# Performance work log

Measured on AMD Instinct MI355X. Metric: run time of the kernel, lower is better.

Reference implementation:

```python
import jax, jax.numpy as jnp
import numpy as np

N_SRC, N_DST, K = 50000, 10000, 32
IN_F, OUT_F, H, L = 256, 128, 8, 10


def setup_inputs() -> dict:
    key = jax.random.key(0)
    ks = jax.random.split(key, 12)
    s = 0.05
    return {
        "feat": jax.random.normal(ks[0], (N_SRC, IN_F), jnp.float32),
        "labels": jax.random.uniform(ks[1], (N_SRC, L), jnp.float32),
        "labels_ori": jax.random.uniform(ks[2], (N_SRC, L), jnp.float32),
        "label_rela": jax.random.uniform(ks[3], (L, L), jnp.float32),
        "W_neigh": jax.random.normal(ks[4], (IN_F, OUT_F), jnp.float32) * s,
        "b_neigh": jnp.zeros((OUT_F,), jnp.float32),
        "W_self": jax.random.normal(ks[5], (IN_F, OUT_F), jnp.float32) * s,
        "b_self": jnp.zeros((OUT_F,), jnp.float32),
        "W_attn": jax.random.normal(ks[6], (2 * OUT_F, OUT_F * H), jnp.float32) * s,
        "b_attn": jnp.zeros((OUT_F * H,), jnp.float32),
        "feat_attn_W": jax.random.normal(ks[7], (1, H, OUT_F), jnp.float32) * s,
        "eps": jnp.full((1,), 0.5, jnp.float32),
        "out_bias": jnp.zeros((OUT_F,), jnp.float32),
        "nbr_idx": jax.random.randint(ks[8], (N_DST, K), 0, N_SRC, jnp.int32),
    }


def reference(feat, labels, labels_ori, label_rela, W_neigh, b_neigh, W_self,
              b_self, W_attn, b_attn, feat_attn_W, eps, out_bias, nbr_idx):
    n_dst = nbr_idx.shape[0]
    # lin_before_mp is True (in_feats > out_feats): fc_neigh applied to src feats
    h_src = feat @ W_neigh + b_neigh                      # (N_SRC, OUT_F)
    feat_dst = feat[:n_dst]
    cent_l = labels[:n_dst]                                # dst predicted labels
    cent_f = h_src[:n_dst]                                 # dst 'f' field
    # mailbox gather: fixed-fanout neighbors
    h = h_src[nbr_idx]                                     # (N, K, OUT_F)
    l_pred = labels[nbr_idx]                               # (N, K, L)
    # label similarity: sum(outer(l_pred_j, cent_l_i) * R)
    label_sim = jnp.einsum('nka,ab,nb->nk', l_pred, label_rela, cent_l)
    # feature attention score
    h_act = jax.nn.leaky_relu(h, negative_slope=0.1)
    cent_rep = jnp.broadcast_to(cent_f[:, None, :], h_act.shape)
    x = jnp.concatenate([h_act, cent_rep], axis=-1)        # (N, K, 2*OUT_F)
    t = (x @ W_attn + b_attn).reshape(n_dst, K, H, OUT_F)
    feat_sim = jnp.einsum('nkhd,hd->nk', t, feat_attn_W[0])
    # merge (torch.tensor(...) in the original detaches this from the graph)
    merge = jax.lax.stop_gradient(label_sim * eps[0] + feat_sim * (1.0 - eps[0]))
    att = jax.nn.softmax(merge, axis=1)                    # (N, K)
    neigh = (h * att[:, :, None]).mean(axis=1)             # (N, OUT_F)
    rst = (feat_dst @ W_self + b_self + neigh) * 0.5 + out_bias
    return rst, cent_l, labels_ori[:n_dst]
```

## Files before the change

### kernel.cpp

```cpp
#include <hip/hip_runtime.h>
#include <hip/hip_bf16.h>

#define N_SRC 50000
#define N_DST 10000
#define KNBR  32
#define IN_F  256
#define OUT_F 128
#define LDIM  10
#define ATTN_OUT 1024
#define NB_BIG  782
#define NB_SELF 157

using f32x4 = __attribute__((ext_vector_type(4))) float;
using s16x8 = __attribute__((ext_vector_type(8))) short;

#define OUT_CENT (N_DST*OUT_F)
#define OUT_LORI (N_DST*OUT_F + N_DST*LDIM)

#define WS_WCOMB 0
#define WS_BN    128
#define WS_BS    (128 + 16384)
#define WS_HSRC  (128 + 32768)
#define WS_SELF0 (128 + 32768 + (N_SRC*OUT_F/2))
#define WS_SCORE (WS_SELF0 + N_DST*OUT_F)

__device__ __forceinline__ ushort f2bf(float x) {
  __hip_bfloat16 h = __float2bfloat16(x);
  return *reinterpret_cast<ushort*>(&h);
}

__global__ __launch_bounds__(256) void prep_kernel(
    const float* __restrict__ W_attn, const float* __restrict__ fW,
    const float* __restrict__ W_neigh, const float* __restrict__ W_self,
    float* __restrict__ w_comb, ushort* __restrict__ Bn, ushort* __restrict__ Bs) {
  const int b = blockIdx.x;
  const int t = threadIdx.x;
  if (b < 128) {
    __shared__ float red[256];
    float s = 0.f;
#pragma unroll
    for (int i = 0; i < 4; ++i) {
      int o = t + i * 256;
      s += W_attn[(size_t)b * ATTN_OUT + o] * fW[o];
    }
    red[t] = s;
    __syncthreads();
    for (int st = 128; st > 0; st >>= 1) {
      if (t < st) red[t] += red[t + st];
      __syncthreads();
    }
    if (t == 0) w_comb[b] = red[0];
  } else if (b < 256) {
    int k = 2 * (b - 128) + (t >> 7);
    int n = t & 127;
    float x = W_neigh[(size_t)k * OUT_F + n];
    Bn[(k >> 3) * 1024 + n * 8 + (k & 7)] = f2bf(x);
  } else {
    int k = 2 * (b - 256) + (t >> 7);
    int n = t & 127;
    float x = W_self[(size_t)k * OUT_F + n];
    Bs[(k >> 3) * 1024 + n * 8 + (k & 7)] = f2bf(x);
  }
}

template<bool OUT_BF16>
__device__ __forceinline__ void gemm_body(
    const float* __restrict__ A, const ushort* __restrict__ Bp,
    const float* __restrict__ bias, const float* __restrict__ w_comb,
    void* __restrict__ C, float* __restrict__ score_f, int M, int m0) {
  const int t = threadIdx.x;
  const int wv = t >> 6, ln = t & 63;
  const int dg = ln & 15, kg = ln >> 4;
  int r = m0 + wv * 16 + dg;
  r = r < M ? r : M - 1;
  const float* arow = &A[(size_t)r * IN_F];

  s16x8 afr[8];
#pragma unroll
  for (int half = 0; half < 2; ++half) {
    f32x4 araw[8];
#pragma unroll
    for (int k0 = 0; k0 < 4; ++k0) {
      const f32x4* ap = (const f32x4*)&arow[(half * 4 + k0) * 32 + kg * 8];
      araw[2 * k0]     = ap[0];
      araw[2 * k0 + 1] = ap[1];
    }
#pragma unroll
    for (int k0 = 0; k0 < 4; ++k0) {
      s16x8 f;
      f[0] = (short)f2bf(araw[2*k0][0]); f[1] = (short)f2bf(araw[2*k0][1]);
      f[2] = (short)f2bf(araw[2*k0][2]); f[3] = (short)f2bf(araw[2*k0][3]);
      f[4] = (short)f2bf(araw[2*k0+1][0]); f[5] = (short)f2bf(araw[2*k0+1][1]);
      f[6] = (short)f2bf(araw[2*k0+1][2]); f[7] = (short)f2bf(araw[2*k0+1][3]);
      afr[half * 4 + k0] = f;
    }
  }

  f32x4 acc[8];
#pragma unroll
  for (int ct = 0; ct < 8; ++ct) acc[ct] = (f32x4){0.f, 0.f, 0.f, 0.f};
#pragma unroll
  for (int k0 = 0; k0 < 8; ++k0) {
    const ushort* bb = Bp + (k0 * 4 + kg) * 1024 + dg * 8;
#pragma unroll
    for (int ct = 0; ct < 8; ++ct) {
      s16x8 bfr = *reinterpret_cast<const s16x8*>(bb + ct * 128);
      acc[ct] = __builtin_amdgcn_mfma_f32_16x16x32_bf16(afr[k0], bfr, acc[ct], 0, 0, 0);
    }
  }

  float sc[4] = {0.f, 0.f, 0.f, 0.f};
#pragma unroll
  for (int ct = 0; ct < 8; ++ct) {
    int col = ct * 16 + dg;
    float bb = bias[col];
    float wc = OUT_BF16 ? w_comb[col] : 0.f;
#pragma unroll
    for (int e = 0; e < 4; ++e) {
      int rr = m0 + wv * 16 + kg * 4 + e;
      float v = acc[ct][e] + bb;
      if (OUT_BF16) {
        sc[e] = fmaf(fmaxf(v, 0.1f * v), wc, sc[e]);
        if (rr < M) ((ushort*)C)[(size_t)rr * OUT_F + col] = f2bf(v);
      } else {
        if (rr < M) ((float*)C)[(size_t)rr * OUT_F + col] = v;
      }
    }
  }
  if (OUT_BF16) {
#pragma unroll
    for (int s = 1; s < 16; s <<= 1) {
#pragma unroll
      for (int e = 0; e < 4; ++e) sc[e] += __shfl_xor(sc[e], s);
    }
    if (dg == 0) {
#pragma unroll
      for (int e = 0; e < 4; ++e) {
        int rr = m0 + wv * 16 + kg * 4 + e;
        if (rr < M) score_f[rr] = sc[e];
      }
    }
  }
}

__global__ __launch_bounds__(256, 4) void fused_gemm(
    const float* __restrict__ A,
    const ushort* __restrict__ Bn, const ushort* __restrict__ Bs,
    const float* __restrict__ bias_n, const float* __restrict__ bias_s,
    const float* __restrict__ w_comb,
    ushort* __restrict__ hsrc, float* __restrict__ self0, float* __restrict__ score_f) {
  if (blockIdx.x < NB_BIG)
    gemm_body<true>(A, Bn, bias_n, w_comb, (void*)hsrc, score_f, N_SRC, blockIdx.x * 64);
  else
    gemm_body<false>(A, Bs, bias_s, w_comb, (void*)self0, score_f, N_DST, (blockIdx.x - NB_BIG) * 64);
}

__global__ __launch_bounds__(256, 4) void attn_kernel(
    const float* __restrict__ labels, const float* __restrict__ labels_ori,
    const float* __restrict__ label_rela, const int* __restrict__ nbr_idx,
    const ushort* __restrict__ hsrc, const float* __restrict__ self0,
    const float* __restrict__ score_f, const float* __restrict__ eps_p,
    const float* __restrict__ out_bias, float* __restrict__ out) {
  const int t = threadIdx.x;
  const int wv = t >> 6, ln = t & 63;
  const int n = blockIdx.x * 4 + wv;
  const int dg = ln & 15, kg = ln >> 4;

  const float eps = eps_p[0];
  const float om = 1.f - eps;

  float va = 0.f;
  if (dg < LDIM) {
#pragma unroll
    for (int b = 0; b < LDIM; ++b)
      va += label_rela[dg * LDIM + b] * labels[(size_t)n * LDIM + b];
    va *= eps;
  }

  const int* irow = nbr_idx + (size_t)n * KNBR;
  int ids[8];
  uint4 hv[8];
#pragma unroll
  for (int j = 0; j < 8; ++j) {
    ids[j] = irow[kg * 8 + j];
    hv[j] = *(const uint4*)(hsrc + (size_t)ids[j] * OUT_F + dg * 8);
  }
  float m[8];
#pragma unroll
  for (int j = 0; j < 8; ++j) {
    float sp = 0.f;
    if (dg == 0) sp = om * score_f[ids[j]];
    if (dg < LDIM) sp = fmaf(labels[(size_t)ids[j] * LDIM + dg], va, sp);
    m[j] = sp;
  }
#pragma unroll
  for (int s = 1; s < 16; s <<= 1) {
#pragma unroll
    for (int j = 0; j < 8; ++j) m[j] += __shfl_xor(m[j], s);
  }
  float mx = m[0];
#pragma unroll
  for (int j = 1; j < 8; ++j) mx = fmaxf(mx, m[j]);
  mx = fmaxf(mx, __shfl_xor(mx, 16));
  mx = fmaxf(mx, __shfl_xor(mx, 32));
  float ssum = 0.f;
#pragma unroll
  for (int j = 0; j < 8; ++j) {
    m[j] = __expf(m[j] - mx);
    ssum += m[j];
  }
  ssum += __shfl_xor(ssum, 16);
  ssum += __shfl_xor(ssum, 32);
  const float scale = 1.f / (ssum * (float)KNBR);
  float pn[8];
#pragma unroll
  for (int e = 0; e < 8; ++e) pn[e] = 0.f;
#pragma unroll
  for (int j = 0; j < 8; ++j) {
    float a = m[j];
    pn[0] = fmaf(a, __uint_as_float(hv[j].x << 16), pn[0]);
    pn[1] = fmaf(a, __uint_as_float(hv[j].x & 0xffff0000u), pn[1]);
    pn[2] = fmaf(a, __uint_as_float(hv[j].y << 16), pn[2]);
    pn[3] = fmaf(a, __uint_as_float(hv[j].y & 0xffff0000u), pn[3]);
    pn[4] = fmaf(a, __uint_as_float(hv[j].z << 16), pn[4]);
    pn[5] = fmaf(a, __uint_as_float(hv[j].z & 0xffff0000u), pn[5]);
    pn[6] = fmaf(a, __uint_as_float(hv[j].w << 16), pn[6]);
    pn[7] = fmaf(a, __uint_as_float(hv[j].w & 0xffff0000u), pn[7]);
  }
#pragma unroll
  for (int e = 0; e < 8; ++e) {
    pn[e] += __shfl_xor(pn[e], 16);
    pn[e] += __shfl_xor(pn[e], 32);
  }
  if (kg == 0) {
    const float* srow = self0 + (size_t)n * OUT_F + dg * 8;
    float* orow = out + (size_t)n * OUT_F + dg * 8;
    f32x4 o0, o1;
#pragma unroll
    for (int e = 0; e < 4; ++e)
      o0[e] = (srow[e] + pn[e] * scale) * 0.5f + out_bias[dg * 8 + e];
#pragma unroll
    for (int e = 0; e < 4; ++e)
      o1[e] = (srow[4 + e] + pn[4 + e] * scale) * 0.5f + out_bias[dg * 8 + 4 + e];
    *(f32x4*)orow = o0;
    *(f32x4*)(orow + 4) = o1;
  }
  if (kg == 1 && dg < LDIM)
    out[OUT_CENT + (size_t)n * LDIM + dg] = labels[(size_t)n * LDIM + dg];
  if (kg == 2 && dg < LDIM)
    out[OUT_LORI + (size_t)n * LDIM + dg] = labels_ori[(size_t)n * LDIM + dg];
}

extern "C" void kernel_launch(void* const* d_in, const int* in_sizes, int n_in,
                              void* d_out, int out_size, void* d_ws, size_t ws_size,
                              hipStream_t stream) {
  const float* feat       = (const float*)d_in[0];
  const float* labels     = (const float*)d_in[1];
  const float* labels_ori = (const float*)d_in[2];
  const float* label_rela = (const float*)d_in[3];
  const float* W_neigh    = (const float*)d_in[4];
  const float* b_neigh    = (const float*)d_in[5];
  const float* W_self     = (const float*)d_in[6];
  const float* b_self     = (const float*)d_in[7];
  const float* W_attn     = (const float*)d_in[8];
  const float* fW         = (const float*)d_in[10];
  const float* eps        = (const float*)d_in[11];
  const float* out_bias   = (const float*)d_in[12];
  const int*   nbr_idx    = (const int*)d_in[13];

  float* wsf = (float*)d_ws;
  float* out = (float*)d_out;

  float*  w_comb  = wsf + WS_WCOMB;
  ushort* Bn      = (ushort*)(wsf + WS_BN);
  ushort* Bsf     = (ushort*)(wsf + WS_BS);
  ushort* h_src   = (ushort*)(wsf + WS_HSRC);
  float*  self0   = wsf + WS_SELF0;
  float*  score_f = wsf + WS_SCORE;

  prep_kernel<<<384, 256, 0, stream>>>(W_attn, fW, W_neigh, W_self, w_comb, Bn, Bsf);
  fused_gemm<<<NB_BIG + NB_SELF, 256, 0, stream>>>(feat, Bn, Bsf, b_neigh, b_self,
                                                   w_comb, h_src, self0, score_f);
  attn_kernel<<<(N_DST / 4), 256, 0, stream>>>(labels, labels_ori, label_rela, nbr_idx,
                                               h_src, self0, score_f, eps, out_bias, out);
}
```

Measured before the change: 59.63 us.

## Split GEMM K dimension across wave pairs with LDS reduction, fold self epilogue

```diff
diff --git a/kernel.cpp b/kernel.cpp
--- a/kernel.cpp
+++ b/kernel.cpp
@@ -8,8 +8,9 @@
 #define OUT_F 128
 #define LDIM  10
 #define ATTN_OUT 1024
-#define NB_BIG  782
-#define NB_SELF 157
+#define NB2_BIG  1563
+#define NB2_SELF 313
+#define NB2_TOT  1876
 
 using f32x4 = __attribute__((ext_vector_type(4))) float;
 using s16x8 = __attribute__((ext_vector_type(8))) short;
@@ -21,12 +22,23 @@
 #define WS_BN    128
 #define WS_BS    (128 + 16384)
 #define WS_HSRC  (128 + 32768)
-#define WS_SELF0 (128 + 32768 + (N_SRC*OUT_F/2))
+#define WS_SELF0 (WS_HSRC + (N_SRC*OUT_F/2))
 #define WS_SCORE (WS_SELF0 + N_DST*OUT_F)
 
 __device__ __forceinline__ ushort f2bf(float x) {
   __hip_bfloat16 h = __float2bfloat16(x);
   return *reinterpret_cast<ushort*>(&h);
+}
+
+__device__ __forceinline__ void unpack8(uint4 hv, float* o) {
+  o[0] = __uint_as_float(hv.x << 16);
+  o[1] = __uint_as_float(hv.x & 0xffff0000u);
+  o[2] = __uint_as_float(hv.y << 16);
+  o[3] = __uint_as_float(hv.y & 0xffff0000u);
+  o[4] = __uint_as_float(hv.z << 16);
+  o[5] = __uint_as_float(hv.z & 0xffff0000u);
+  o[6] = __uint_as_float(hv.w << 16);
+  o[7] = __uint_as_float(hv.w & 0xffff0000u);
 }
 
 __global__ __launch_bounds__(256) void prep_kernel(
@@ -53,55 +65,52 @@
   } else if (b < 256) {
     int k = 2 * (b - 128) + (t >> 7);
     int n = t & 127;
-    float x = W_neigh[(size_t)k * OUT_F + n];
-    Bn[(k >> 3) * 1024 + n * 8 + (k & 7)] = f2bf(x);
+    Bn[(k >> 3) * 1024 + n * 8 + (k & 7)] = f2bf(W_neigh[(size_t)k * OUT_F + n]);
   } else {
     int k = 2 * (b - 256) + (t >> 7);
     int n = t & 127;
-    float x = W_self[(size_t)k * OUT_F + n];
-    Bs[(k >> 3) * 1024 + n * 8 + (k & 7)] = f2bf(x);
-  }
-}
-
-template<bool OUT_BF16>
-__device__ __forceinline__ void gemm_body(
-    const float* __restrict__ A, const ushort* __restrict__ Bp,
-    const float* __restrict__ bias, const float* __restrict__ w_comb,
-    void* __restrict__ C, float* __restrict__ score_f, int M, int m0) {
+    Bs[(k >> 3) * 1024 + n * 8 + (k & 7)] = f2bf(W_self[(size_t)k * OUT_F + n]);
+  }
+}
+
+template<bool NEIGH, bool SCORE>
+__device__ __forceinline__ void gemm_tile_ks(
+    const float* A, const ushort* Bp, const float* bias,
+    const float* out_bias, const float* w_comb, float* score_f,
+    void* C, int M, int m0) {
+  __shared__ f32x4 lred[2][64][8];
   const int t = threadIdx.x;
   const int wv = t >> 6, ln = t & 63;
+  const int grp = wv >> 1, half = wv & 1;
   const int dg = ln & 15, kg = ln >> 4;
-  int r = m0 + wv * 16 + dg;
+  int r = m0 + grp * 16 + dg;
   r = r < M ? r : M - 1;
-  const float* arow = &A[(size_t)r * IN_F];
-
-  s16x8 afr[8];
-#pragma unroll
-  for (int half = 0; half < 2; ++half) {
-    f32x4 araw[8];
-#pragma unroll
-    for (int k0 = 0; k0 < 4; ++k0) {
-      const f32x4* ap = (const f32x4*)&arow[(half * 4 + k0) * 32 + kg * 8];
-      araw[2 * k0]     = ap[0];
-      araw[2 * k0 + 1] = ap[1];
-    }
-#pragma unroll
-    for (int k0 = 0; k0 < 4; ++k0) {
-      s16x8 f;
-      f[0] = (short)f2bf(araw[2*k0][0]); f[1] = (short)f2bf(araw[2*k0][1]);
-      f[2] = (short)f2bf(araw[2*k0][2]); f[3] = (short)f2bf(araw[2*k0][3]);
-      f[4] = (short)f2bf(araw[2*k0+1][0]); f[5] = (short)f2bf(araw[2*k0+1][1]);
-      f[6] = (short)f2bf(araw[2*k0+1][2]); f[7] = (short)f2bf(araw[2*k0+1][3]);
-      afr[half * 4 + k0] = f;
-    }
+  const float* arow = &A[(size_t)r * IN_F + half * 128];
+
+  f32x4 araw[8];
+#pragma unroll
+  for (int k0 = 0; k0 < 4; ++k0) {
+    const f32x4* ap = (const f32x4*)&arow[k0 * 32 + kg * 8];
+    araw[2 * k0]     = ap[0];
+    araw[2 * k0 + 1] = ap[1];
+  }
+  s16x8 afr[4];
+#pragma unroll
+  for (int k0 = 0; k0 < 4; ++k0) {
+    s16x8 f;
+    f[0] = (short)f2bf(araw[2*k0][0]); f[1] = (short)f2bf(araw[2*k0][1]);
+    f[2] = (short)f2bf(araw[2*k0][2]); f[3] = (short)f2bf(araw[2*k0][3]);
+    f[4] = (short)f2bf(araw[2*k0+1][0]); f[5] = (short)f2bf(araw[2*k0+1][1]);
+    f[6] = (short)f2bf(araw[2*k0+1][2]); f[7] = (short)f2bf(araw[2*k0+1][3]);
+    afr[k0] = f;
   }
 
   f32x4 acc[8];
 #pragma unroll
   for (int ct = 0; ct < 8; ++ct) acc[ct] = (f32x4){0.f, 0.f, 0.f, 0.f};
 #pragma unroll
-  for (int k0 = 0; k0 < 8; ++k0) {
-    const ushort* bb = Bp + (k0 * 4 + kg) * 1024 + dg * 8;
+  for (int k0 = 0; k0 < 4; ++k0) {
+    const ushort* bb = Bp + (size_t)(half * 16 + k0 * 4 + kg) * 1024 + dg * 8;
 #pragma unroll
     for (int ct = 0; ct < 8; ++ct) {
       s16x8 bfr = *reinterpret_cast<const s16x8*>(bb + ct * 128);
@@ -109,35 +118,47 @@
     }
   }
 
-  float sc[4] = {0.f, 0.f, 0.f, 0.f};
-#pragma unroll
-  for (int ct = 0; ct < 8; ++ct) {
-    int col = ct * 16 + dg;
-    float bb = bias[col];
-    float wc = OUT_BF16 ? w_comb[col] : 0.f;
-#pragma unroll
-    for (int e = 0; e < 4; ++e) {
-      int rr = m0 + wv * 16 + kg * 4 + e;
-      float v = acc[ct][e] + bb;
-      if (OUT_BF16) {
-        sc[e] = fmaf(fmaxf(v, 0.1f * v), wc, sc[e]);
-        if (rr < M) ((ushort*)C)[(size_t)rr * OUT_F + col] = f2bf(v);
-      } else {
-        if (rr < M) ((float*)C)[(size_t)rr * OUT_F + col] = v;
+  if (half == 0) {
+#pragma unroll
+    for (int ct = 0; ct < 8; ++ct) lred[grp][ln][ct] = acc[ct];
+  }
+  __syncthreads();
+  if (half == 1) {
+#pragma unroll
+    for (int ct = 0; ct < 8; ++ct) {
+      f32x4 o = lred[grp][ln][ct];
+#pragma unroll
+      for (int e = 0; e < 4; ++e) acc[ct][e] += o[e];
+    }
+    float sc[4] = {0.f, 0.f, 0.f, 0.f};
+#pragma unroll
+    for (int ct = 0; ct < 8; ++ct) {
+      int col = ct * 16 + dg;
+      float bb = bias[col];
+      float wc = SCORE ? w_comb[col] : 0.f;
+#pragma unroll
+      for (int e = 0; e < 4; ++e) {
+        int rr = m0 + grp * 16 + kg * 4 + e;
+        float v = acc[ct][e] + bb;
+        if (SCORE) sc[e] = fmaf(fmaxf(v, 0.1f * v), wc, sc[e]);
+        if (rr < M) {
+          if (NEIGH) ((ushort*)C)[(size_t)rr * OUT_F + col] = f2bf(v);
+          else       ((float*)C)[(size_t)rr * OUT_F + col] = v * 0.5f + out_bias[col];
+        }
       }
     }
-  }
-  if (OUT_BF16) {
-#pragma unroll
-    for (int s = 1; s < 16; s <<= 1) {
-#pragma unroll
-      for (int e = 0; e < 4; ++e) sc[e] += __shfl_xor(sc[e], s);
-    }
-    if (dg == 0) {
-#pragma unroll
-      for (int e = 0; e < 4; ++e) {
-        int rr = m0 + wv * 16 + kg * 4 + e;
-        if (rr < M) score_f[rr] = sc[e];
+    if (SCORE) {
+#pragma unroll
+      for (int s = 1; s < 16; s <<= 1) {
+#pragma unroll
+        for (int e = 0; e < 4; ++e) sc[e] += __shfl_xor(sc[e], s);
+      }
+      if (dg == 0) {
+#pragma unroll
+        for (int e = 0; e < 4; ++e) {
+          int rr = m0 + grp * 16 + kg * 4 + e;
+          if (rr < M) score_f[rr] = sc[e];
+        }
       }
     }
   }
@@ -147,12 +168,14 @@
     const float* __restrict__ A,
     const ushort* __restrict__ Bn, const ushort* __restrict__ Bs,
     const float* __restrict__ bias_n, const float* __restrict__ bias_s,
-    const float* __restrict__ w_comb,
+    const float* __restrict__ w_comb, const float* __restrict__ out_bias,
     ushort* __restrict__ hsrc, float* __restrict__ self0, float* __restrict__ score_f) {
-  if (blockIdx.x < NB_BIG)
-    gemm_body<true>(A, Bn, bias_n, w_comb, (void*)hsrc, score_f, N_SRC, blockIdx.x * 64);
+  if (blockIdx.x < NB2_BIG)
+    gemm_tile_ks<true, true>(A, Bn, bias_n, out_bias, w_comb, score_f,
+                             (void*)hsrc, N_SRC, blockIdx.x * 32);
   else
-    gemm_body<false>(A, Bs, bias_s, w_comb, (void*)self0, score_f, N_DST, (blockIdx.x - NB_BIG) * 64);
+    gemm_tile_ks<false, false>(A, Bs, bias_s, out_bias, nullptr, nullptr,
+                               (void*)self0, N_DST, (blockIdx.x - NB2_BIG) * 32);
 }
 
 __global__ __launch_bounds__(256, 4) void attn_kernel(
@@ -211,21 +234,17 @@
   }
   ssum += __shfl_xor(ssum, 16);
   ssum += __shfl_xor(ssum, 32);
-  const float scale = 1.f / (ssum * (float)KNBR);
+  const float scale2 = 0.5f / (ssum * (float)KNBR);
   float pn[8];
 #pragma unroll
   for (int e = 0; e < 8; ++e) pn[e] = 0.f;
 #pragma unroll
   for (int j = 0; j < 8; ++j) {
     float a = m[j];
-    pn[0] = fmaf(a, __uint_as_float(hv[j].x << 16), pn[0]);
-    pn[1] = fmaf(a, __uint_as_float(hv[j].x & 0xffff0000u), pn[1]);
-    pn[2] = fmaf(a, __uint_as_float(hv[j].y << 16), pn[2]);
-    pn[3] = fmaf(a, __uint_as_float(hv[j].y & 0xffff0000u), pn[3]);
-    pn[4] = fmaf(a, __uint_as_float(hv[j].z << 16), pn[4]);
-    pn[5] = fmaf(a, __uint_as_float(hv[j].z & 0xffff0000u), pn[5]);
-    pn[6] = fmaf(a, __uint_as_float(hv[j].w << 16), pn[6]);
-    pn[7] = fmaf(a, __uint_as_float(hv[j].w & 0xffff0000u), pn[7]);
+    float hfj[8];
+    unpack8(hv[j], hfj);
+#pragma unroll
+    for (int e = 0; e < 8; ++e) pn[e] = fmaf(a, hfj[e], pn[e]);
   }
 #pragma unroll
   for (int e = 0; e < 8; ++e) {
@@ -237,11 +256,9 @@
     float* orow = out + (size_t)n * OUT_F + dg * 8;
     f32x4 o0, o1;
 #pragma unroll
-    for (int e = 0; e < 4; ++e)
-      o0[e] = (srow[e] + pn[e] * scale) * 0.5f + out_bias[dg * 8 + e];
-#pragma unroll
-    for (int e = 0; e < 4; ++e)
-      o1[e] = (srow[4 + e] + pn[4 + e] * scale) * 0.5f + out_bias[dg * 8 + 4 + e];
+    for (int e = 0; e < 4; ++e) o0[e] = fmaf(pn[e], scale2, srow[e]);
+#pragma unroll
+    for (int e = 0; e < 4; ++e) o1[e] = fmaf(pn[4 + e], scale2, srow[4 + e]);
     *(f32x4*)orow = o0;
     *(f32x4*)(orow + 4) = o1;
   }
@@ -279,8 +296,8 @@
   float*  score_f = wsf + WS_SCORE;
 
   prep_kernel<<<384, 256, 0, stream>>>(W_attn, fW, W_neigh, W_self, w_comb, Bn, Bsf);
-  fused_gemm<<<NB_BIG + NB_SELF, 256, 0, stream>>>(feat, Bn, Bsf, b_neigh, b_self,
-                                                   w_comb, h_src, self0, score_f);
+  fused_gemm<<<NB2_TOT, 256, 0, stream>>>(feat, Bn, Bsf, b_neigh, b_self,
+                                          w_comb, out_bias, h_src, self0, score_f);
   attn_kernel<<<(N_DST / 4), 256, 0, stream>>>(labels, labels_ori, label_rela, nbr_idx,
                                                h_src, self0, score_f, eps, out_bias, out);
 }
```

After: 62.20 us (median of 2 runs). +4.3%, slower.
